# Kernel optimization log

Hardware: AMD Instinct MI355X
Metric: run time of the kernel (lower is better)

Reference implementation:

```python
import jax, jax.numpy as jnp
import numpy as np

DIM = 1024
HEADS = 8
DIM_HEAD = 64
EPS = 1e-10
LN_EPS = 1e-5


def setup_inputs() -> dict:
    key = jax.random.key(0)
    k1, k2, k3 = jax.random.split(key, 3)
    b, n = 2, 4096
    x = jax.random.normal(k1, (b, n, DIM), dtype=jnp.float32)
    ln_gamma = jnp.ones((DIM,), dtype=jnp.float32)
    ln_beta = jnp.zeros((DIM,), dtype=jnp.float32)
    w_qkv = jax.random.normal(k2, (DIM, 3 * HEADS * DIM_HEAD), dtype=jnp.float32) * (DIM ** -0.5)
    w_out = jax.random.normal(k3, (HEADS * DIM_HEAD, DIM), dtype=jnp.float32) * ((HEADS * DIM_HEAD) ** -0.5)
    return {"x": x, "ln_gamma": ln_gamma, "ln_beta": ln_beta, "w_qkv": w_qkv, "w_out": w_out}


def _layernorm(x, gamma, beta):
    mu = jnp.mean(x, axis=-1, keepdims=True)
    var = jnp.var(x, axis=-1, keepdims=True)
    return (x - mu) * jax.lax.rsqrt(var + LN_EPS) * gamma + beta


def reference(x, ln_gamma, ln_beta, w_qkv, w_out):
    b, n, _ = x.shape
    h, dh = HEADS, DIM_HEAD
    scale = dh ** -0.5

    xn = _layernorm(x, ln_gamma, ln_beta)          # prenorm
    qkv = xn @ w_qkv                               # [b, n, 3*h*dh]
    q, k, v = jnp.split(qkv, 3, axis=-1)
    # [b, n, h*dh] -> [b, h, n, dh]
    def to_heads(t):
        return t.reshape(b, n, h, dh).transpose(0, 2, 1, 3)
    q, k, v = to_heads(q), to_heads(k), to_heads(v)

    # Ring/blockwise attention with online softmax is mathematically
    # equivalent to full softmax attention with an eps in the denominator.
    sim = jnp.einsum('bhid,bhjd->bhij', q, k) * scale   # [b, h, n, n]
    causal_mask = jnp.tril(jnp.ones((n, n), dtype=bool))
    sim = jnp.where(causal_mask, sim, -jnp.finfo(sim.dtype).max)

    m = jnp.max(sim, axis=-1, keepdims=True)            # row max (stable)
    p = jnp.exp(sim - m)
    denom = jnp.sum(p, axis=-1, keepdims=True) + EPS
    attn = p / denom

    out = jnp.einsum('bhij,bhjd->bhid', attn, v)        # [b, h, n, dh]
    out = out.transpose(0, 2, 1, 3).reshape(b, n, h * dh)
    return out @ w_out                                  # [b, n, dim]
```

## Files before the change

### kernel.cpp

```cpp
#include <hip/hip_runtime.h>
#include <hip/hip_bf16.h>
#include <stdint.h>

typedef unsigned short u16;
typedef unsigned int u32;

typedef __attribute__((ext_vector_type(8))) __bf16 bf16x8;
typedef __attribute__((ext_vector_type(4))) float f32x4;
typedef __attribute__((ext_vector_type(8))) u16 u16x8;

#define DIM 1024
#define SEQ 4096
#define NTOK 8192
#define NBH 16
#define NSLOT 96

static __device__ __forceinline__ float bf2f(u16 u) {
    union { u32 u; float f; } c; c.u = ((u32)u) << 16; return c.f;
}
static __device__ __forceinline__ u16 f2bf(float f) {
    union { float f; u32 u; } c; c.f = f;
    u32 u = c.u;
    return (u16)((u + 0x7FFF + ((u >> 16) & 1)) >> 16);
}
static __device__ __forceinline__ u16 cvt_bf16(float f) {
    union { __bf16 b; u16 u; } c; c.b = (__bf16)f;
    return c.u;
}
static __device__ __forceinline__ f32x4 mfma_bf16(bf16x8 a, bf16x8 b, f32x4 c) {
    return __builtin_amdgcn_mfma_f32_16x16x32_bf16(a, b, c, 0, 0, 0);
}

typedef const __attribute__((address_space(1))) unsigned int* gptr_t;
typedef __attribute__((address_space(3))) unsigned int* lptr_t;

__global__ __launch_bounds__(256) void ln_kernel(const float* __restrict__ x,
                                                 const float* __restrict__ g,
                                                 const float* __restrict__ bta,
                                                 u16* __restrict__ xn) {
    int row = blockIdx.x;
    int tid = threadIdx.x;
    float4 v = ((const float4*)(x + (size_t)row * DIM))[tid];
    float f[4] = {v.x, v.y, v.z, v.w};
    float s = 0.f, s2 = 0.f;
#pragma unroll
    for (int i = 0; i < 4; i++) { s += f[i]; s2 += f[i] * f[i]; }
#pragma unroll
    for (int m = 1; m < 64; m <<= 1) { s += __shfl_xor(s, m); s2 += __shfl_xor(s2, m); }
    __shared__ float red[8];
    int w = tid >> 6;
    if ((tid & 63) == 0) { red[w * 2] = s; red[w * 2 + 1] = s2; }
    __syncthreads();
    s  = red[0] + red[2] + red[4] + red[6];
    s2 = red[1] + red[3] + red[5] + red[7];
    float mu = s * (1.f / DIM);
    float var = s2 * (1.f / DIM) - mu * mu;
    float rstd = rsqrtf(var + 1e-5f);
    u16 o[4];
#pragma unroll
    for (int i = 0; i < 4; i++) {
        int c = tid * 4 + i;
        o[i] = f2bf((f[i] - mu) * rstd * g[c] + bta[c]);
    }
    *(uint64_t*)(xn + (size_t)row * DIM + tid * 4) = *(uint64_t*)o;
}

__global__ __launch_bounds__(256) void transpose_kernel(const float* __restrict__ src,
                                                        u16* __restrict__ dst,
                                                        int R, int C) {
    __shared__ float t[32][33];
    int lx = threadIdx.x & 31, ly = threadIdx.x >> 5;
    int c = blockIdx.x * 32 + lx;
#pragma unroll
    for (int i = 0; i < 32; i += 8)
        t[ly + i][lx] = src[(size_t)(blockIdx.y * 32 + ly + i) * C + c];
    __syncthreads();
    int rr = blockIdx.y * 32 + lx;
#pragma unroll
    for (int i = 0; i < 32; i += 8)
        dst[(size_t)(blockIdx.x * 32 + ly + i) * R + rr] = f2bf(t[lx][ly + i]);
}

template <int K>
static __device__ __forceinline__ void gemm_core(const u16* __restrict__ A,
                                                 const u16* __restrict__ B,
                                                 int rowBase, int colBase,
                                                 u16* A_lds, u16* B_lds,
                                                 f32x4 acc[4][4]) {
    int tid = threadIdx.x;
    int lane = tid & 63;
    int l15 = lane & 15, q4 = lane >> 4;
    int w = tid >> 6;
    int wm = w >> 1, wn = w & 1;
#pragma unroll
    for (int mt = 0; mt < 4; mt++)
#pragma unroll
        for (int nt = 0; nt < 4; nt++) acc[mt][nt] = (f32x4){0.f, 0.f, 0.f, 0.f};

    char* Ab = (char*)A_lds;
    char* Bb = (char*)B_lds;

    for (int k0 = 0; k0 < K; k0 += 32) {
        __syncthreads();
#pragma unroll
        for (int i = 0; i < 2; i++) {
            int c = i * 256 + tid;
            int r = c >> 2;
            int piece = (c & 3) * 8;
            const u16* gA = A + (size_t)(rowBase + r) * K + k0 + piece;
            const u16* gB = B + (size_t)(colBase + r) * K + k0 + piece;
            unsigned ldsOff = (unsigned)(i * 4096 + w * 1024);
            __builtin_amdgcn_global_load_lds((gptr_t)gA, (lptr_t)(Ab + ldsOff), 16, 0, 0);
            __builtin_amdgcn_global_load_lds((gptr_t)gB, (lptr_t)(Bb + ldsOff), 16, 0, 0);
        }
        __syncthreads();
        bf16x8 a[4], b[4];
#pragma unroll
        for (int mt = 0; mt < 4; mt++)
            a[mt] = *(const bf16x8*)(A_lds + (wm * 64 + mt * 16 + l15) * 32 + q4 * 8);
#pragma unroll
        for (int nt = 0; nt < 4; nt++)
            b[nt] = *(const bf16x8*)(B_lds + (wn * 64 + nt * 16 + l15) * 32 + q4 * 8);
#pragma unroll
        for (int mt = 0; mt < 4; mt++)
#pragma unroll
            for (int nt = 0; nt < 4; nt++)
                acc[mt][nt] = mfma_bf16(a[mt], b[nt], acc[mt][nt]);
    }
}

__global__ __launch_bounds__(256) void gemm_qkv_kernel(const u16* __restrict__ xn,
                                                       const u16* __restrict__ wT,
                                                       u16* __restrict__ qb,
                                                       u16* __restrict__ kb,
                                                       u16* __restrict__ vbT) {
    __shared__ u16 A_lds[128 * 32];
    __shared__ u16 B_lds[128 * 32];
    f32x4 acc[4][4];
    gemm_core<1024>(xn, wT, blockIdx.x * 128, blockIdx.y * 128, A_lds, B_lds, acc);
    int lane = threadIdx.x & 63;
    int w = threadIdx.x >> 6;
    int wm = w >> 1, wn = w & 1;
    const float SC = 0.125f * 1.44269504f;
#pragma unroll
    for (int mt = 0; mt < 4; mt++) {
#pragma unroll
        for (int nt = 0; nt < 4; nt++) {
#pragma unroll
            for (int r = 0; r < 4; r++) {
                int m = blockIdx.x * 128 + wm * 64 + mt * 16 + (lane >> 4) * 4 + r;
                int n = blockIdx.y * 128 + wn * 64 + nt * 16 + (lane & 15);
                int piece = n >> 9;
                int c = n & 511;
                int h = c >> 6;
                int d = c & 63;
                int bi = m >> 12;
                int nn = m & 4095;
                int bh = bi * 8 + h;
                float av = acc[mt][nt][r];
                if (piece == 0)      qb[((size_t)(bh * SEQ + nn) << 6) + d] = f2bf(av * SC);
                else if (piece == 1) kb[((size_t)(bh * SEQ + nn) << 6) + d] = f2bf(av);
                else                 vbT[((size_t)(bh * 64 + d) << 12) + nn] = f2bf(av);
            }
        }
    }
}

__global__ __launch_bounds__(256) void gemm_out_kernel(const u16* __restrict__ aout,
                                                       const u16* __restrict__ wT,
                                                       float* __restrict__ out) {
    __shared__ u16 A_lds[128 * 32];
    __shared__ u16 B_lds[128 * 32];
    f32x4 acc[4][4];
    gemm_core<512>(aout, wT, blockIdx.x * 128, blockIdx.y * 128, A_lds, B_lds, acc);
    int lane = threadIdx.x & 63;
    int w = threadIdx.x >> 6;
    int wm = w >> 1, wn = w & 1;
#pragma unroll
    for (int mt = 0; mt < 4; mt++) {
#pragma unroll
        for (int nt = 0; nt < 4; nt++) {
#pragma unroll
            for (int r = 0; r < 4; r++) {
                int m = blockIdx.x * 128 + wm * 64 + mt * 16 + (lane >> 4) * 4 + r;
                int n = blockIdx.y * 128 + wn * 64 + nt * 16 + (lane & 15);
                out[(size_t)m * DIM + n] = acc[mt][nt][r];
            }
        }
    }
}

#define ASTR 72

__global__ __launch_bounds__(256) void attn_partial_kernel(const u16* __restrict__ qb,
                                                           const u16* __restrict__ kb,
                                                           const u16* __restrict__ vbT,
                                                           u16* __restrict__ part,
                                                           float* __restrict__ lpart) {
    __shared__ u16 K_lds[64 * ASTR];
    __shared__ u16 VT_lds[64 * ASTR];
    __shared__ u16 QP_lds[64 * ASTR];

    int idx = NBH * NSLOT - 1 - blockIdx.x;
    int bh = idx / NSLOT;
    int s  = idx - bh * NSLOT;
    int qt, ci;
    if (s < 32) { qt = s; ci = 0; }
    else        { int t = s - 32; qt = 32 + (t >> 1); ci = t & 1; }
    int kt0 = ci * 32;
    int kt1 = min(kt0 + 31, qt);

    int tid = threadIdx.x;
    int lane = tid & 63;
    int l15 = lane & 15, q4 = lane >> 4;
    int w = tid >> 6;

    const u16* Qp  = qb + ((size_t)bh * SEQ + qt * 64) * 64;
    const u16* Kp0 = kb + (size_t)bh * SEQ * 64;
    const u16* VTp = vbT + ((size_t)bh * 64) * SEQ;

#pragma unroll
    for (int i = 0; i < 2; i++) {
        int c = tid + 256 * i;
        int r = c >> 3;
        int kc = (c & 7) * 8;
        *(u16x8*)(QP_lds + r * ASTR + kc) = *(const u16x8*)(Qp + r * 64 + kc);
    }
    __syncthreads();
    bf16x8 aQ0 = *(const bf16x8*)(QP_lds + (w * 16 + l15) * ASTR + q4 * 8);
    bf16x8 aQ1 = *(const bf16x8*)(QP_lds + (w * 16 + l15) * ASTR + 32 + q4 * 8);
    __syncthreads();

    f32x4 Oacc[4];
    f32x4 l_acc = (f32x4){0.f, 0.f, 0.f, 0.f};
#pragma unroll
    for (int vt = 0; vt < 4; vt++) Oacc[vt] = (f32x4){0.f, 0.f, 0.f, 0.f};

    const __bf16 one_bf = (__bf16)1.0f;
    bf16x8 vones = {one_bf, one_bf, one_bf, one_bf, one_bf, one_bf, one_bf, one_bf};

    u16* Pw = QP_lds + w * 16 * ASTR;

    int c0 = tid, c1 = tid + 256;
    int r0 = c0 >> 3, kc0 = (c0 & 7) * 8;
    int r1 = c1 >> 3, kc1 = (c1 & 7) * 8;

    u16x8 krA0, krA1, vrA0, vrA1;
    {
        const u16* Kp = Kp0 + (size_t)kt0 * 64 * 64;
        krA0 = *(const u16x8*)(Kp + r0 * 64 + kc0);
        krA1 = *(const u16x8*)(Kp + r1 * 64 + kc1);
        vrA0 = *(const u16x8*)(VTp + (size_t)r0 * SEQ + kt0 * 64 + kc0);
        vrA1 = *(const u16x8*)(VTp + (size_t)r1 * SEQ + kt0 * 64 + kc1);
    }

    for (int kt = kt0; kt <= kt1; kt++) {
        __syncthreads();
        *(u16x8*)(K_lds + r0 * ASTR + kc0) = krA0;
        *(u16x8*)(K_lds + r1 * ASTR + kc1) = krA1;
        *(u16x8*)(VT_lds + r0 * ASTR + kc0) = vrA0;
        *(u16x8*)(VT_lds + r1 * ASTR + kc1) = vrA1;
        int ktn = (kt < kt1) ? kt + 1 : kt1;
        const u16* Kpn = Kp0 + (size_t)ktn * 64 * 64;
        u16x8 krB0 = *(const u16x8*)(Kpn + r0 * 64 + kc0);
        u16x8 krB1 = *(const u16x8*)(Kpn + r1 * 64 + kc1);
        u16x8 vrB0 = *(const u16x8*)(VTp + (size_t)r0 * SEQ + ktn * 64 + kc0);
        u16x8 vrB1 = *(const u16x8*)(VTp + (size_t)r1 * SEQ + ktn * 64 + kc1);
        __syncthreads();

        f32x4 sv[4];
#pragma unroll
        for (int nt = 0; nt < 4; nt++) {
            bf16x8 b0 = *(const bf16x8*)(K_lds + (nt * 16 + l15) * ASTR + q4 * 8);
            bf16x8 b1 = *(const bf16x8*)(K_lds + (nt * 16 + l15) * ASTR + 32 + q4 * 8);
            f32x4 z = (f32x4){0.f, 0.f, 0.f, 0.f};
            z = mfma_bf16(aQ0, b0, z);
            z = mfma_bf16(aQ1, b1, z);
            sv[nt] = z;
        }

        if (kt != qt) {
#pragma unroll
            for (int nt = 0; nt < 4; nt++)
#pragma unroll
                for (int r = 0; r < 4; r++)
                    Pw[(q4 * 4 + r) * ASTR + nt * 16 + l15] =
                        cvt_bf16(__builtin_amdgcn_exp2f(sv[nt][r]));
        } else {
#pragma unroll
            for (int nt = 0; nt < 4; nt++)
#pragma unroll
                for (int r = 0; r < 4; r++) {
                    int kg = nt * 16 + l15;
                    int qg = w * 16 + q4 * 4 + r;
                    float pv = (kg <= qg) ? __builtin_amdgcn_exp2f(sv[nt][r]) : 0.f;
                    Pw[(q4 * 4 + r) * ASTR + nt * 16 + l15] = cvt_bf16(pv);
                }
        }

        bf16x8 aP0 = *(const bf16x8*)(Pw + l15 * ASTR + q4 * 8);
        bf16x8 aP1 = *(const bf16x8*)(Pw + l15 * ASTR + 32 + q4 * 8);
        l_acc = mfma_bf16(aP0, vones, l_acc);
        l_acc = mfma_bf16(aP1, vones, l_acc);
#pragma unroll
        for (int vt = 0; vt < 4; vt++) {
            bf16x8 bV0 = *(const bf16x8*)(VT_lds + (vt * 16 + l15) * ASTR + q4 * 8);
            bf16x8 bV1 = *(const bf16x8*)(VT_lds + (vt * 16 + l15) * ASTR + 32 + q4 * 8);
            Oacc[vt] = mfma_bf16(aP0, bV0, Oacc[vt]);
            Oacc[vt] = mfma_bf16(aP1, bV1, Oacc[vt]);
        }

        krA0 = krB0; krA1 = krB1; vrA0 = vrB0; vrA1 = vrB1;
    }

    u16* po = part + (size_t)idx * 4096;
#pragma unroll
    for (int vt = 0; vt < 4; vt++)
#pragma unroll
        for (int r = 0; r < 4; r++) {
            int q = w * 16 + q4 * 4 + r;
            int d = vt * 16 + l15;
            po[q * 64 + d] = f2bf(Oacc[vt][r]);
        }
    if (l15 == 0) {
#pragma unroll
        for (int r = 0; r < 4; r++)
            lpart[(size_t)idx * 64 + w * 16 + q4 * 4 + r] = l_acc[r];
    }
}

__global__ __launch_bounds__(256) void attn_combine_kernel(const u16* __restrict__ part,
                                                           const float* __restrict__ lpart,
                                                           u16* __restrict__ aout) {
    int bid = blockIdx.x;
    int bh = bid >> 6;
    int qt = bid & 63;
    int nc = 1 + (qt >> 5);
    int sb = bh * NSLOT + (qt < 32 ? qt : 32 + (qt - 32) * 2);

    int t = threadIdx.x;
    int q = t >> 2;
    int dg = (t & 3) * 16;

    float acc[16];
#pragma unroll
    for (int j = 0; j < 16; j++) acc[j] = 0.f;
    float ll = 0.f;
    for (int ci = 0; ci < nc; ci++) {
        const u16* pp = part + (size_t)(sb + ci) * 4096 + q * 64 + dg;
        u16x8 v0 = *(const u16x8*)pp;
        u16x8 v1 = *(const u16x8*)(pp + 8);
#pragma unroll
        for (int j = 0; j < 8; j++) { acc[j] += bf2f(v0[j]); acc[8 + j] += bf2f(v1[j]); }
        ll += lpart[(size_t)(sb + ci) * 64 + q];
    }
    float inv = 1.f / (ll + 1e-10f);
    int b = bh >> 3, h = bh & 7;
    size_t row = (size_t)(b * SEQ + qt * 64 + q);
    u16 o[16];
#pragma unroll
    for (int j = 0; j < 16; j++) o[j] = f2bf(acc[j] * inv);
    u16* dst = aout + row * 512 + h * 64 + dg;
    *(u16x8*)dst = *(u16x8*)o;
    *(u16x8*)(dst + 8) = *(u16x8*)(o + 8);
}

extern "C" void kernel_launch(void* const* d_in, const int* in_sizes, int n_in,
                              void* d_out, int out_size, void* d_ws, size_t ws_size,
                              hipStream_t stream) {
    const float* x    = (const float*)d_in[0];
    const float* g    = (const float*)d_in[1];
    const float* bta  = (const float*)d_in[2];
    const float* wqkv = (const float*)d_in[3];
    const float* wout = (const float*)d_in[4];
    float* out = (float*)d_out;

    char* ws = (char*)d_ws;
    size_t off = 0;
    auto alloc = [&](size_t bytes) {
        void* p = ws + off;
        off += (bytes + 255) & ~(size_t)255;
        return p;
    };
    u16* xn    = (u16*)alloc((size_t)NTOK * DIM * 2);
    u16* wqkvT = (u16*)alloc((size_t)1536 * 1024 * 2);
    u16* woutT = (u16*)alloc((size_t)1024 * 512 * 2);
    u16* qb    = (u16*)alloc((size_t)NBH * SEQ * 64 * 2);
    u16* kb    = (u16*)alloc((size_t)NBH * SEQ * 64 * 2);
    u16* vbT   = (u16*)alloc((size_t)NBH * SEQ * 64 * 2);
    u16* part  = xn;
    float* lpart = (float*)(xn + (size_t)NBH * NSLOT * 4096);
    u16* aout  = qb;

    ln_kernel<<<NTOK, 256, 0, stream>>>(x, g, bta, xn);
    transpose_kernel<<<dim3(1536 / 32, 1024 / 32), 256, 0, stream>>>(wqkv, wqkvT, 1024, 1536);
    transpose_kernel<<<dim3(1024 / 32, 512 / 32), 256, 0, stream>>>(wout, woutT, 512, 1024);
    gemm_qkv_kernel<<<dim3(64, 12), 256, 0, stream>>>(xn, wqkvT, qb, kb, vbT);
    attn_partial_kernel<<<NBH * NSLOT, 256, 0, stream>>>(qb, kb, vbT, part, lpart);
    attn_combine_kernel<<<NBH * 64, 256, 0, stream>>>(part, lpart, aout);
    gemm_out_kernel<<<dim3(64, 8), 256, 0, stream>>>(aout, woutT, out);
}
```

Measured before the change: 245.8 us.

## Split keys across waves with register-resident Q/K/V and LDS reduction in attention

The attention partial kernel is restructured so each wave owns a 16-key slice of every 64-key tile and all 64 queries, loading Q, K and V fragments straight from global memory into registers. This drops the per-tile LDS staging and the two barriers per iteration. P is kept in registers in transposed form and fed to an fp16 16x16x16 MFMA against V, which is now stored as fp16, and the row sums are taken in registers instead of through an MFMA against a ones vector. The per-wave partial outputs are rounded to bf16 and summed through LDS at the end. In exchange there are more scattered uncoalesced global loads, larger accumulator register pressure, and extra rounding steps.

```diff
diff --git a/kernel.cpp b/kernel.cpp
--- a/kernel.cpp
+++ b/kernel.cpp
@@ -6,7 +6,9 @@
 typedef unsigned int u32;
 
 typedef __attribute__((ext_vector_type(8))) __bf16 bf16x8;
+typedef __attribute__((ext_vector_type(4))) _Float16 f16x4;
 typedef __attribute__((ext_vector_type(4))) float f32x4;
+typedef __attribute__((ext_vector_type(4))) u16 u16x4;
 typedef __attribute__((ext_vector_type(8))) u16 u16x8;
 
 #define DIM 1024
@@ -15,6 +17,8 @@
 #define NBH 16
 #define NSLOT 96
 
+#define MFMA16X16F16 __builtin_amdgcn_mfma_f32_16x16x16f16
+
 static __device__ __forceinline__ float bf2f(u16 u) {
     union { u32 u; float f; } c; c.u = ((u32)u) << 16; return c.f;
 }
@@ -23,9 +27,8 @@
     u32 u = c.u;
     return (u16)((u + 0x7FFF + ((u >> 16) & 1)) >> 16);
 }
-static __device__ __forceinline__ u16 cvt_bf16(float f) {
-    union { __bf16 b; u16 u; } c; c.b = (__bf16)f;
-    return c.u;
+static __device__ __forceinline__ u16 f2h(float f) {
+    union { _Float16 h; u16 u; } c; c.h = (_Float16)f; return c.u;
 }
 static __device__ __forceinline__ f32x4 mfma_bf16(bf16x8 a, bf16x8 b, f32x4 c) {
     return __builtin_amdgcn_mfma_f32_16x16x32_bf16(a, b, c, 0, 0, 0);
@@ -160,7 +163,7 @@
                 float av = acc[mt][nt][r];
                 if (piece == 0)      qb[((size_t)(bh * SEQ + nn) << 6) + d] = f2bf(av * SC);
                 else if (piece == 1) kb[((size_t)(bh * SEQ + nn) << 6) + d] = f2bf(av);
-                else                 vbT[((size_t)(bh * 64 + d) << 12) + nn] = f2bf(av);
+                else                 vbT[((size_t)(bh * 64 + d) << 12) + nn] = f2h(av);
             }
         }
     }
@@ -190,16 +193,13 @@
     }
 }
 
-#define ASTR 72
-
 __global__ __launch_bounds__(256) void attn_partial_kernel(const u16* __restrict__ qb,
                                                            const u16* __restrict__ kb,
                                                            const u16* __restrict__ vbT,
                                                            u16* __restrict__ part,
                                                            float* __restrict__ lpart) {
-    __shared__ u16 K_lds[64 * ASTR];
-    __shared__ u16 VT_lds[64 * ASTR];
-    __shared__ u16 QP_lds[64 * ASTR];
+    __shared__ u16 redO[4 * 64 * 72];
+    __shared__ float redL[4 * 64];
 
     int idx = NBH * NSLOT - 1 - blockIdx.x;
     int bh = idx / NSLOT;
@@ -209,124 +209,128 @@
     else        { int t = s - 32; qt = 32 + (t >> 1); ci = t & 1; }
     int kt0 = ci * 32;
     int kt1 = min(kt0 + 31, qt);
+    int nsteps = kt1 - kt0 + 1;
 
     int tid = threadIdx.x;
     int lane = tid & 63;
     int l15 = lane & 15, q4 = lane >> 4;
     int w = tid >> 6;
 
-    const u16* Qp  = qb + ((size_t)bh * SEQ + qt * 64) * 64;
-    const u16* Kp0 = kb + (size_t)bh * SEQ * 64;
-    const u16* VTp = vbT + ((size_t)bh * 64) * SEQ;
-
-#pragma unroll
-    for (int i = 0; i < 2; i++) {
-        int c = tid + 256 * i;
-        int r = c >> 3;
-        int kc = (c & 7) * 8;
-        *(u16x8*)(QP_lds + r * ASTR + kc) = *(const u16x8*)(Qp + r * 64 + kc);
+    const u16* Qb = qb + ((size_t)(bh * SEQ + qt * 64)) * 64;
+    const u16* Kb = kb + (size_t)bh * SEQ * 64;
+    const u16* Vb = vbT + (size_t)bh * 64 * SEQ;
+
+    bf16x8 Qf[4][2];
+#pragma unroll
+    for (int qtile = 0; qtile < 4; qtile++)
+#pragma unroll
+        for (int dc = 0; dc < 2; dc++)
+            Qf[qtile][dc] = *(const bf16x8*)(Qb + (size_t)(qtile * 16 + l15) * 64 + dc * 32 + q4 * 8);
+
+    f32x4 Oacc[4][4];
+#pragma unroll
+    for (int dt = 0; dt < 4; dt++)
+#pragma unroll
+        for (int qtile = 0; qtile < 4; qtile++) Oacc[dt][qtile] = (f32x4){0.f, 0.f, 0.f, 0.f};
+    float l_acc[4] = {0.f, 0.f, 0.f, 0.f};
+
+    int key0 = kt0 * 64 + w * 16;
+    bf16x8 kf0, kf1, kn0, kn1;
+    f16x4 vf[4], vn[4];
+    kf0 = *(const bf16x8*)(Kb + (size_t)(key0 + l15) * 64 + q4 * 8);
+    kf1 = *(const bf16x8*)(Kb + (size_t)(key0 + l15) * 64 + 32 + q4 * 8);
+#pragma unroll
+    for (int dt = 0; dt < 4; dt++)
+        vf[dt] = *(const f16x4*)(Vb + (size_t)(dt * 16 + l15) * SEQ + key0 + q4 * 4);
+
+    for (int i = 0; i < nsteps; i++) {
+        int keyn = key0 + min(i + 1, nsteps - 1) * 64;
+        kn0 = *(const bf16x8*)(Kb + (size_t)(keyn + l15) * 64 + q4 * 8);
+        kn1 = *(const bf16x8*)(Kb + (size_t)(keyn + l15) * 64 + 32 + q4 * 8);
+#pragma unroll
+        for (int dt = 0; dt < 4; dt++)
+            vn[dt] = *(const f16x4*)(Vb + (size_t)(dt * 16 + l15) * SEQ + keyn + q4 * 4);
+
+        if (kt0 + i != qt) {
+#pragma unroll
+            for (int qtile = 0; qtile < 4; qtile++) {
+                f32x4 z = (f32x4){0.f, 0.f, 0.f, 0.f};
+                z = mfma_bf16(kf0, Qf[qtile][0], z);
+                z = mfma_bf16(kf1, Qf[qtile][1], z);
+                f16x4 pf;
+#pragma unroll
+                for (int r = 0; r < 4; r++) {
+                    float pv = __builtin_amdgcn_exp2f(z[r]);
+                    l_acc[qtile] += pv;
+                    pf[r] = (_Float16)pv;
+                }
+#pragma unroll
+                for (int dt = 0; dt < 4; dt++)
+                    Oacc[dt][qtile] = MFMA16X16F16(vf[dt], pf, Oacc[dt][qtile], 0, 0, 0);
+            }
+        } else {
+#pragma unroll
+            for (int qtile = 0; qtile < 4; qtile++) {
+                f32x4 z = (f32x4){0.f, 0.f, 0.f, 0.f};
+                z = mfma_bf16(kf0, Qf[qtile][0], z);
+                z = mfma_bf16(kf1, Qf[qtile][1], z);
+                f16x4 pf;
+#pragma unroll
+                for (int r = 0; r < 4; r++) {
+                    float pv = (w * 16 + q4 * 4 + r <= qtile * 16 + l15)
+                                   ? __builtin_amdgcn_exp2f(z[r]) : 0.f;
+                    l_acc[qtile] += pv;
+                    pf[r] = (_Float16)pv;
+                }
+#pragma unroll
+                for (int dt = 0; dt < 4; dt++)
+                    Oacc[dt][qtile] = MFMA16X16F16(vf[dt], pf, Oacc[dt][qtile], 0, 0, 0);
+            }
+        }
+        kf0 = kn0; kf1 = kn1;
+#pragma unroll
+        for (int dt = 0; dt < 4; dt++) vf[dt] = vn[dt];
+    }
+
+#pragma unroll
+    for (int qtile = 0; qtile < 4; qtile++) {
+#pragma unroll
+        for (int dt = 0; dt < 4; dt++) {
+            u16 pk[4];
+#pragma unroll
+            for (int r = 0; r < 4; r++) pk[r] = f2bf(Oacc[dt][qtile][r]);
+            *(uint64_t*)(redO + (size_t)(w * 64 + qtile * 16 + l15) * 72 + dt * 16 + q4 * 4) =
+                *(uint64_t*)pk;
+        }
+        float l = l_acc[qtile];
+        l += __shfl_xor(l, 16);
+        l += __shfl_xor(l, 32);
+        if (q4 == 0) redL[w * 64 + qtile * 16 + l15] = l;
     }
     __syncthreads();
-    bf16x8 aQ0 = *(const bf16x8*)(QP_lds + (w * 16 + l15) * ASTR + q4 * 8);
-    bf16x8 aQ1 = *(const bf16x8*)(QP_lds + (w * 16 + l15) * ASTR + 32 + q4 * 8);
-    __syncthreads();
-
-    f32x4 Oacc[4];
-    f32x4 l_acc = (f32x4){0.f, 0.f, 0.f, 0.f};
-#pragma unroll
-    for (int vt = 0; vt < 4; vt++) Oacc[vt] = (f32x4){0.f, 0.f, 0.f, 0.f};
-
-    const __bf16 one_bf = (__bf16)1.0f;
-    bf16x8 vones = {one_bf, one_bf, one_bf, one_bf, one_bf, one_bf, one_bf, one_bf};
-
-    u16* Pw = QP_lds + w * 16 * ASTR;
-
-    int c0 = tid, c1 = tid + 256;
-    int r0 = c0 >> 3, kc0 = (c0 & 7) * 8;
-    int r1 = c1 >> 3, kc1 = (c1 & 7) * 8;
-
-    u16x8 krA0, krA1, vrA0, vrA1;
-    {
-        const u16* Kp = Kp0 + (size_t)kt0 * 64 * 64;
-        krA0 = *(const u16x8*)(Kp + r0 * 64 + kc0);
-        krA1 = *(const u16x8*)(Kp + r1 * 64 + kc1);
-        vrA0 = *(const u16x8*)(VTp + (size_t)r0 * SEQ + kt0 * 64 + kc0);
-        vrA1 = *(const u16x8*)(VTp + (size_t)r1 * SEQ + kt0 * 64 + kc1);
-    }
-
-    for (int kt = kt0; kt <= kt1; kt++) {
-        __syncthreads();
-        *(u16x8*)(K_lds + r0 * ASTR + kc0) = krA0;
-        *(u16x8*)(K_lds + r1 * ASTR + kc1) = krA1;
-        *(u16x8*)(VT_lds + r0 * ASTR + kc0) = vrA0;
-        *(u16x8*)(VT_lds + r1 * ASTR + kc1) = vrA1;
-        int ktn = (kt < kt1) ? kt + 1 : kt1;
-        const u16* Kpn = Kp0 + (size_t)ktn * 64 * 64;
-        u16x8 krB0 = *(const u16x8*)(Kpn + r0 * 64 + kc0);
-        u16x8 krB1 = *(const u16x8*)(Kpn + r1 * 64 + kc1);
-        u16x8 vrB0 = *(const u16x8*)(VTp + (size_t)r0 * SEQ + ktn * 64 + kc0);
-        u16x8 vrB1 = *(const u16x8*)(VTp + (size_t)r1 * SEQ + ktn * 64 + kc1);
-        __syncthreads();
-
-        f32x4 sv[4];
-#pragma unroll
-        for (int nt = 0; nt < 4; nt++) {
-            bf16x8 b0 = *(const bf16x8*)(K_lds + (nt * 16 + l15) * ASTR + q4 * 8);
-            bf16x8 b1 = *(const bf16x8*)(K_lds + (nt * 16 + l15) * ASTR + 32 + q4 * 8);
-            f32x4 z = (f32x4){0.f, 0.f, 0.f, 0.f};
-            z = mfma_bf16(aQ0, b0, z);
-            z = mfma_bf16(aQ1, b1, z);
-            sv[nt] = z;
-        }
-
-        if (kt != qt) {
-#pragma unroll
-            for (int nt = 0; nt < 4; nt++)
-#pragma unroll
-                for (int r = 0; r < 4; r++)
-                    Pw[(q4 * 4 + r) * ASTR + nt * 16 + l15] =
-                        cvt_bf16(__builtin_amdgcn_exp2f(sv[nt][r]));
-        } else {
-#pragma unroll
-            for (int nt = 0; nt < 4; nt++)
-#pragma unroll
-                for (int r = 0; r < 4; r++) {
-                    int kg = nt * 16 + l15;
-                    int qg = w * 16 + q4 * 4 + r;
-                    float pv = (kg <= qg) ? __builtin_amdgcn_exp2f(sv[nt][r]) : 0.f;
-                    Pw[(q4 * 4 + r) * ASTR + nt * 16 + l15] = cvt_bf16(pv);
-                }
-        }
-
-        bf16x8 aP0 = *(const bf16x8*)(Pw + l15 * ASTR + q4 * 8);
-        bf16x8 aP1 = *(const bf16x8*)(Pw + l15 * ASTR + 32 + q4 * 8);
-        l_acc = mfma_bf16(aP0, vones, l_acc);
-        l_acc = mfma_bf16(aP1, vones, l_acc);
-#pragma unroll
-        for (int vt = 0; vt < 4; vt++) {
-            bf16x8 bV0 = *(const bf16x8*)(VT_lds + (vt * 16 + l15) * ASTR + q4 * 8);
-            bf16x8 bV1 = *(const bf16x8*)(VT_lds + (vt * 16 + l15) * ASTR + 32 + q4 * 8);
-            Oacc[vt] = mfma_bf16(aP0, bV0, Oacc[vt]);
-            Oacc[vt] = mfma_bf16(aP1, bV1, Oacc[vt]);
-        }
-
-        krA0 = krB0; krA1 = krB1; vrA0 = vrB0; vrA1 = vrB1;
-    }
-
-    u16* po = part + (size_t)idx * 4096;
-#pragma unroll
-    for (int vt = 0; vt < 4; vt++)
-#pragma unroll
-        for (int r = 0; r < 4; r++) {
-            int q = w * 16 + q4 * 4 + r;
-            int d = vt * 16 + l15;
-            po[q * 64 + d] = f2bf(Oacc[vt][r]);
-        }
-    if (l15 == 0) {
-#pragma unroll
-        for (int r = 0; r < 4; r++)
-            lpart[(size_t)idx * 64 + w * 16 + q4 * 4 + r] = l_acc[r];
-    }
+
+    int q = tid >> 2;
+    int ds = (tid & 3) * 16;
+    float acc[16];
+#pragma unroll
+    for (int j = 0; j < 16; j++) acc[j] = 0.f;
+    float ll = 0.f;
+#pragma unroll
+    for (int w2 = 0; w2 < 4; w2++) {
+        const u16* pr = redO + (size_t)(w2 * 64 + q) * 72 + ds;
+        u16x8 a0 = *(const u16x8*)pr;
+        u16x8 a1 = *(const u16x8*)(pr + 8);
+#pragma unroll
+        for (int j = 0; j < 8; j++) { acc[j] += bf2f(a0[j]); acc[8 + j] += bf2f(a1[j]); }
+        ll += redL[w2 * 64 + q];
+    }
+    u16 o[16];
+#pragma unroll
+    for (int j = 0; j < 16; j++) o[j] = f2bf(acc[j]);
+    u16* po = part + (size_t)idx * 4096 + q * 64 + ds;
+    *(u16x8*)po = *(u16x8*)o;
+    *(u16x8*)(po + 8) = *(u16x8*)(o + 8);
+    if ((tid & 3) == 0) lpart[(size_t)idx * 64 + q] = ll;
 }
 
 __global__ __launch_bounds__(256) void attn_combine_kernel(const u16* __restrict__ part,
```

Measured after the change: 296.4 us. +20.6%, slower.
